# Kernel optimization log

Hardware: AMD Instinct MI355X
Metric: run time of the kernel (lower is better)

Reference implementation:

```python
import jax, jax.numpy as jnp
import numpy as np

NHEAD = 8
DILATED = 1


def setup_inputs() -> dict:
    key = jax.random.key(0)
    ks = jax.random.split(key, 5)
    bs, c, h, w, k = 2, 256, 128, 128, 8
    L = (h // 2) * (w // 2)
    return {
        "query": jax.random.normal(ks[0], (bs, c, h, w), jnp.float32),
        "key": jax.random.normal(ks[1], (bs, c, h, w), jnp.float32),
        "value": jax.random.normal(ks[2], (bs, c, h, w), jnp.float32),
        "topk_pos": jax.random.randint(ks[3], (bs, L, k, 2), 0, h // 2, dtype=jnp.int32).astype(jnp.int64),
        "rel_pos": jax.random.normal(ks[4], (bs, NHEAD, h, w, 4 * k), jnp.float32),
    }


def reference(query, key, value, topk_pos, rel_pos):
    bs, c, h0, w0 = query.shape
    h1, w1 = key.shape[2], key.shape[3]
    nh = NHEAD
    d = c // nh
    L = (h0 // 2) * (w0 // 2)
    k = topk_pos.shape[2]
    k4 = 4 * k

    # key/value: [b,c,h,w] -> [b, h1*w1, nh, d]
    kf = key.reshape(bs, c, h1 * w1).transpose(0, 2, 1).reshape(bs, h1 * w1, nh, d)
    vf = value.reshape(bs, c, h1 * w1).transpose(0, 2, 1).reshape(bs, h1 * w1, nh, d)

    # query grouped into 2x2 blocks: [b, L, 4, nh, d]
    q = query.reshape(bs, nh, d, h0 // 2, 2, w0 // 2, 2)
    q = q.transpose(0, 3, 5, 4, 6, 1, 2).reshape(bs, L, 4, nh, d)

    # build gather indices into flattened key grid (offsets by dilation)
    tp = topk_pos * 2                               # [b, L, k, 2]
    row, col = tp[..., 0], tp[..., 1]
    offs = [(0, 0), (0, DILATED), (DILATED, 0), (DILATED, DILATED)]
    idx = jnp.stack([(row + x) * w1 + (col + y) for x, y in offs], axis=3)  # [b,L,k,4]
    idx = jnp.clip(idx, 0, h1 * w1 - 1).reshape(bs, L, k4)

    def gather(tbl):  # tbl: [b, h1*w1, nh, d] -> [b, L, k4, nh, d]
        return jax.vmap(lambda t, i: t[i])(tbl, idx.reshape(bs, L * k4)).reshape(bs, L, k4, nh, d)

    kg = gather(kf)
    vg = gather(vf)

    scale = 1.0 / np.sqrt(d).astype(np.float32)
    qk = jnp.einsum('blthd,blmhd->bltmh', q, kg) * scale  # [b,L,4,k4,nh]

    rp = rel_pos.reshape(bs, nh, h0 // 2, 2, w0 // 2, 2, k4)
    rp = rp.transpose(0, 2, 4, 3, 5, 6, 1).reshape(bs, L, 4, k4, nh)
    qk = qk + rp

    A = jax.nn.softmax(qk, axis=-2)  # softmax over the k*4 candidate axis
    msg = jnp.einsum('bltmh,blmhd->blthd', A, vg)  # [b,L,4,nh,d]

    # un-group 2x2 blocks back to full resolution: [b, h0*w0, c]
    msg = msg.reshape(bs, h0 // 2, w0 // 2, 2, 2, nh, d)
    msg = msg.transpose(0, 1, 3, 2, 4, 5, 6).reshape(bs, h0 * w0, c)

    up_idx = jnp.broadcast_to(idx[:, :, None, :], (bs, L, 4, k4))
    up_idx = up_idx.reshape(bs, h0 // 2, w0 // 2, 2, 2, k4)
    up_idx = up_idx.transpose(0, 1, 3, 2, 4, 5).reshape(bs, h0 * w0, k4)
    return msg, up_idx
```

## Files before the change

kernel.cpp:

```cpp
#include <hip/hip_runtime.h>
#include <math.h>

constexpr int NH = 8;
constexpr int D = 32;
constexpr int C = 256;
constexpr int H0 = 128;
constexpr int W0 = 128;
constexpr int PIX = H0 * W0;
constexpr int LBLK = 4096;
constexpr int K4 = 32;
constexpr int KST = 258;

__global__ __launch_bounds__(256) void transpose_qkv_kernel(
    const float* __restrict__ q, const float* __restrict__ k,
    const float* __restrict__ v, float* __restrict__ ws)
{
  __shared__ float tile[64][65];
  const int arr = blockIdx.z >> 1;
  const int b = blockIdx.z & 1;
  const float* src = (arr == 0 ? q : arr == 1 ? k : v) + (size_t)b * C * PIX;
  float* dst = ws + (size_t)arr * 2 * PIX * C + (size_t)b * PIX * C;

  const int p0 = blockIdx.x * 64;
  const int c0 = blockIdx.y * 64;
  const int tx = threadIdx.x & 63;
  const int ty = threadIdx.x >> 6;

#pragma unroll
  for (int r = 0; r < 16; ++r) {
    const int ch = ty + r * 4;
    tile[ch][tx] = src[(size_t)(c0 + ch) * PIX + p0 + tx];
  }
  __syncthreads();
#pragma unroll
  for (int r = 0; r < 16; ++r) {
    const int prow = ty + r * 4;
    dst[(size_t)(p0 + prow) * C + c0 + tx] = tile[tx][prow];
  }
}

__global__ __launch_bounds__(256) void cascade_attn_kernel(
    const float* __restrict__ qT,
    const float* __restrict__ kT,
    const float* __restrict__ vT,
    const int* __restrict__ topk,
    const float* __restrict__ relp,
    float* __restrict__ out_msg,
    float* __restrict__ out_idx)
{
  __shared__ float kv[K4 * KST];
  __shared__ float qs[4 * C];
  __shared__ float as_[NH * K4 * 4];

  const int tid = threadIdx.x;
  const int bid = blockIdx.x;
  const int b = bid >> 12;
  const int l = bid & (LBLK - 1);
  const int by = l >> 6, bx = l & 63;
  const int r0 = by * 2, c0 = bx * 2;

  const int* tp = topk + ((size_t)b * LBLK + l) * 16;

  {
    const int t = tid >> 6, ln = tid & 63;
    const int pix = r0 * W0 + c0 + (t >> 1) * W0 + (t & 1);
    float4 f = *(const float4*)&qT[((size_t)b * PIX + pix) * C + ln * 4];
    *(float4*)&qs[t * C + ln * 4] = f;
  }

  const int p = tid >> 3;
  const int ln8 = tid & 7;
  const int jj = p >> 2, o = p & 3;
  const int gpix = (tp[jj * 2] * 2 + (o >> 1)) * W0 + tp[jj * 2 + 1] * 2 + (o & 1);

  {
    const float* src = &kT[((size_t)b * PIX + gpix) * C + ln8 * 4];
#pragma unroll
    for (int i = 0; i < 8; ++i) {
      float4 f = *(const float4*)(src + i * 32);
      float* dst = &kv[p * KST + ln8 * 4 + i * 32];
      ((float2*)dst)[0] = make_float2(f.x, f.y);
      ((float2*)(dst + 2))[0] = make_float2(f.z, f.w);
    }
  }

  float4 vreg[8];
  {
    const float* src = &vT[((size_t)b * PIX + gpix) * C + ln8 * 4];
#pragma unroll
    for (int i = 0; i < 8; ++i) vreg[i] = *(const float4*)(src + i * 32);
  }

  if (tid < 128) {
    const int m = tid & 31, t = tid >> 5;
    const int j2 = m >> 2, o2 = m & 3;
    const int pix = (tp[j2 * 2] * 2 + (o2 >> 1)) * W0 + tp[j2 * 2 + 1] * 2 + (o2 & 1);
    const int prow = r0 + (t >> 1), pcol = c0 + (t & 1);
    out_idx[((size_t)b * PIX + prow * W0 + pcol) * K4 + m] = (float)pix;
  }
  __syncthreads();

  const int h = tid >> 5;
  const int m = tid & 31;

  float a0 = 0.f, a1 = 0.f, a2 = 0.f, a3 = 0.f;
#pragma unroll
  for (int dq = 0; dq < 8; ++dq) {
    const int off = h * D + dq * 4;
    float4 q0 = *(const float4*)&qs[0 * C + off];
    float4 q1 = *(const float4*)&qs[1 * C + off];
    float4 q2 = *(const float4*)&qs[2 * C + off];
    float4 q3 = *(const float4*)&qs[3 * C + off];
    float2 ka = *(const float2*)&kv[m * KST + off];
    float2 kc = *(const float2*)&kv[m * KST + off + 2];
    a0 += q0.x * ka.x + q0.y * ka.y + q0.z * kc.x + q0.w * kc.y;
    a1 += q1.x * ka.x + q1.y * ka.y + q1.z * kc.x + q1.w * kc.y;
    a2 += q2.x * ka.x + q2.y * ka.y + q2.z * kc.x + q2.w * kc.y;
    a3 += q3.x * ka.x + q3.y * ka.y + q3.z * kc.x + q3.w * kc.y;
  }

  const float scale = 0.17677669529663687f;
  const size_t rb = ((((size_t)b * NH + h) * H0 + r0) * W0 + c0) * K4 + m;
  float sv[4];
  sv[0] = a0 * scale + relp[rb];
  sv[1] = a1 * scale + relp[rb + K4];
  sv[2] = a2 * scale + relp[rb + (size_t)W0 * K4];
  sv[3] = a3 * scale + relp[rb + (size_t)W0 * K4 + K4];

  float pr4[4];
#pragma unroll
  for (int t = 0; t < 4; ++t) {
    float x = sv[t];
    float mx = x;
#pragma unroll
    for (int off = 16; off > 0; off >>= 1) mx = fmaxf(mx, __shfl_xor(mx, off));
    float pbit = __expf(x - mx);
    float sm = pbit;
#pragma unroll
    for (int off = 16; off > 0; off >>= 1) sm += __shfl_xor(sm, off);
    pr4[t] = pbit / sm;
  }
  *(float4*)&as_[tid * 4] = make_float4(pr4[0], pr4[1], pr4[2], pr4[3]);
  __syncthreads();

#pragma unroll
  for (int i = 0; i < 8; ++i) {
    float* dst = &kv[p * KST + ln8 * 4 + i * 32];
    ((float2*)dst)[0] = make_float2(vreg[i].x, vreg[i].y);
    ((float2*)(dst + 2))[0] = make_float2(vreg[i].z, vreg[i].w);
  }
  __syncthreads();

  float o0 = 0.f, o1 = 0.f, o2 = 0.f, o3 = 0.f;
#pragma unroll
  for (int mm = 0; mm < 32; ++mm) {
    float4 a4 = *(const float4*)&as_[(h * K4 + mm) * 4];
    float vv = kv[mm * KST + h * D + m];
    o0 += a4.x * vv;
    o1 += a4.y * vv;
    o2 += a4.z * vv;
    o3 += a4.w * vv;
  }
  const size_t ob = ((size_t)b * PIX + (size_t)r0 * W0 + c0) * C + h * D + m;
  out_msg[ob] = o0;
  out_msg[ob + C] = o1;
  out_msg[ob + (size_t)W0 * C] = o2;
  out_msg[ob + (size_t)W0 * C + C] = o3;
}

__global__ __launch_bounds__(256) void cascade_attn_fallback(
    const float* __restrict__ query, const float* __restrict__ key,
    const float* __restrict__ value, const int* __restrict__ topk,
    const float* __restrict__ relp, float* __restrict__ out_msg,
    float* __restrict__ out_idx)
{
  __shared__ float kv[K4 * KST];
  __shared__ float qs[4 * C];
  __shared__ float as_[NH * K4 * 4];

  const int tid = threadIdx.x;
  const int bid = blockIdx.x;
  const int b = bid >> 12;
  const int l = bid & (LBLK - 1);
  const int by = l >> 6, bx = l & 63;
  const int r0 = by * 2, c0 = bx * 2;

  const size_t plane = (size_t)PIX;
  const float* qb = query + (size_t)b * C * plane;
  const float* kb = key + (size_t)b * C * plane;
  const float* vb = value + (size_t)b * C * plane;
  const int* tp = topk + ((size_t)b * LBLK + l) * 16;

  {
    const float* qp = qb + (size_t)tid * plane + r0 * W0 + c0;
    float2 a = *(const float2*)qp;
    float2 bb = *(const float2*)(qp + W0);
    qs[0 * C + tid] = a.x; qs[1 * C + tid] = a.y;
    qs[2 * C + tid] = bb.x; qs[3 * C + tid] = bb.y;
  }
#pragma unroll
  for (int it = 0; it < 16; ++it) {
    const int jj = it >> 1, x = it & 1;
    const int pr = tp[jj * 2] * 2 + x;
    const int pc = tp[jj * 2 + 1] * 2;
    float2 f = *(const float2*)(kb + (size_t)tid * plane + pr * W0 + pc);
    const int m0 = jj * 4 + x * 2;
    kv[m0 * KST + tid] = f.x;
    kv[(m0 + 1) * KST + tid] = f.y;
  }
  if (tid < 128) {
    const int m = tid & 31, t = tid >> 5;
    const int jj = m >> 2, o = m & 3;
    const int pix = (tp[jj * 2] * 2 + (o >> 1)) * W0 + tp[jj * 2 + 1] * 2 + (o & 1);
    const int prow = r0 + (t >> 1), pcol = c0 + (t & 1);
    out_idx[((size_t)b * plane + prow * W0 + pcol) * K4 + m] = (float)pix;
  }
  __syncthreads();

  const int h = tid >> 5;
  const int m = tid & 31;
  float a0 = 0.f, a1 = 0.f, a2 = 0.f, a3 = 0.f;
#pragma unroll
  for (int dq = 0; dq < 8; ++dq) {
    const int off = h * D + dq * 4;
    float4 q0 = *(const float4*)&qs[0 * C + off];
    float4 q1 = *(const float4*)&qs[1 * C + off];
    float4 q2 = *(const float4*)&qs[2 * C + off];
    float4 q3 = *(const float4*)&qs[3 * C + off];
    float2 ka = *(const float2*)&kv[m * KST + off];
    float2 kc = *(const float2*)&kv[m * KST + off + 2];
    a0 += q0.x * ka.x + q0.y * ka.y + q0.z * kc.x + q0.w * kc.y;
    a1 += q1.x * ka.x + q1.y * ka.y + q1.z * kc.x + q1.w * kc.y;
    a2 += q2.x * ka.x + q2.y * ka.y + q2.z * kc.x + q2.w * kc.y;
    a3 += q3.x * ka.x + q3.y * ka.y + q3.z * kc.x + q3.w * kc.y;
  }
  const float scale = 0.17677669529663687f;
  const size_t rb = ((((size_t)b * NH + h) * H0 + r0) * W0 + c0) * K4 + m;
  float sv[4];
  sv[0] = a0 * scale + relp[rb];
  sv[1] = a1 * scale + relp[rb + K4];
  sv[2] = a2 * scale + relp[rb + (size_t)W0 * K4];
  sv[3] = a3 * scale + relp[rb + (size_t)W0 * K4 + K4];
  float pr4[4];
#pragma unroll
  for (int t = 0; t < 4; ++t) {
    float x = sv[t];
    float mx = x;
#pragma unroll
    for (int off = 16; off > 0; off >>= 1) mx = fmaxf(mx, __shfl_xor(mx, off));
    float pbit = __expf(x - mx);
    float sm = pbit;
#pragma unroll
    for (int off = 16; off > 0; off >>= 1) sm += __shfl_xor(sm, off);
    pr4[t] = pbit / sm;
  }
  *(float4*)&as_[tid * 4] = make_float4(pr4[0], pr4[1], pr4[2], pr4[3]);
  __syncthreads();
#pragma unroll
  for (int it = 0; it < 16; ++it) {
    const int jj = it >> 1, x = it & 1;
    const int pr = tp[jj * 2] * 2 + x;
    const int pc = tp[jj * 2 + 1] * 2;
    float2 f = *(const float2*)(vb + (size_t)tid * plane + pr * W0 + pc);
    const int m0 = jj * 4 + x * 2;
    kv[m0 * KST + tid] = f.x;
    kv[(m0 + 1) * KST + tid] = f.y;
  }
  __syncthreads();
  float o0 = 0.f, o1 = 0.f, o2 = 0.f, o3 = 0.f;
#pragma unroll
  for (int mm = 0; mm < 32; ++mm) {
    float4 a4 = *(const float4*)&as_[(h * K4 + mm) * 4];
    float vv = kv[mm * KST + h * D + m];
    o0 += a4.x * vv; o1 += a4.y * vv; o2 += a4.z * vv; o3 += a4.w * vv;
  }
  const size_t ob = ((size_t)b * plane + (size_t)r0 * W0 + c0) * C + h * D + m;
  out_msg[ob] = o0;
  out_msg[ob + C] = o1;
  out_msg[ob + (size_t)W0 * C] = o2;
  out_msg[ob + (size_t)W0 * C + C] = o3;
}

extern "C" void kernel_launch(void* const* d_in, const int* in_sizes, int n_in,
                              void* d_out, int out_size, void* d_ws, size_t ws_size,
                              hipStream_t stream) {
  const float* q = (const float*)d_in[0];
  const float* k = (const float*)d_in[1];
  const float* v = (const float*)d_in[2];
  const int* tp = (const int*)d_in[3];
  const float* rp = (const float*)d_in[4];

  float* out_msg = (float*)d_out;
  float* out_idx = out_msg + (size_t)2 * PIX * C;

  const size_t needed = (size_t)3 * 2 * PIX * C * sizeof(float);
  if (ws_size >= needed) {
    float* ws = (float*)d_ws;
    float* qT = ws;
    float* kT = ws + (size_t)2 * PIX * C;
    float* vT = ws + (size_t)4 * PIX * C;
    dim3 tg(PIX / 64, C / 64, 6);
    hipLaunchKernelGGL(transpose_qkv_kernel, tg, dim3(256), 0, stream, q, k, v, ws);
    hipLaunchKernelGGL(cascade_attn_kernel, dim3(2 * LBLK), dim3(256), 0, stream,
                       qT, kT, vT, tp, rp, out_msg, out_idx);
  } else {
    hipLaunchKernelGGL(cascade_attn_fallback, dim3(2 * LBLK), dim3(256), 0, stream,
                       q, k, v, tp, rp, out_msg, out_idx);
  }
}
```

Baseline: 247.7 us.

## Vectorize transpose with float4, prefetch rel_pos early, reuse query smem for probs

The transpose kernel now moves data with float4 global loads and stores and scatters them into a padded shared tile, cutting the number of memory instructions. In the attention kernel the rel_pos loads are issued before the first barrier so their latency overlaps the K/V gathers. The softmax probabilities now overwrite the query shared buffer instead of using a separate array, which lowers shared memory per block and may raise occupancy. The transpose scatter writes into shared memory may incur bank conflicts, and the strided scalar reads of the tile are assembled into float4 stores.

```diff
diff --git a/kernel.cpp b/kernel.cpp
--- a/kernel.cpp
+++ b/kernel.cpp
@@ -15,7 +15,7 @@
     const float* __restrict__ q, const float* __restrict__ k,
     const float* __restrict__ v, float* __restrict__ ws)
 {
-  __shared__ float tile[64][65];
+  __shared__ float tile[64 * 65];
   const int arr = blockIdx.z >> 1;
   const int b = blockIdx.z & 1;
   const float* src = (arr == 0 ? q : arr == 1 ? k : v) + (size_t)b * C * PIX;
@@ -23,19 +23,27 @@
 
   const int p0 = blockIdx.x * 64;
   const int c0 = blockIdx.y * 64;
-  const int tx = threadIdx.x & 63;
-  const int ty = threadIdx.x >> 6;
-
-#pragma unroll
-  for (int r = 0; r < 16; ++r) {
-    const int ch = ty + r * 4;
-    tile[ch][tx] = src[(size_t)(c0 + ch) * PIX + p0 + tx];
-  }
-  __syncthreads();
-#pragma unroll
-  for (int r = 0; r < 16; ++r) {
-    const int prow = ty + r * 4;
-    dst[(size_t)(p0 + prow) * C + c0 + tx] = tile[tx][prow];
+  const int t15 = threadIdx.x & 15;
+  const int thi = threadIdx.x >> 4;
+
+#pragma unroll
+  for (int r = 0; r < 4; ++r) {
+    const int ch = thi + r * 16;
+    const int p4 = t15 * 4;
+    float4 f = *(const float4*)&src[(size_t)(c0 + ch) * PIX + p0 + p4];
+    tile[(p4 + 0) * 65 + ch] = f.x;
+    tile[(p4 + 1) * 65 + ch] = f.y;
+    tile[(p4 + 2) * 65 + ch] = f.z;
+    tile[(p4 + 3) * 65 + ch] = f.w;
+  }
+  __syncthreads();
+#pragma unroll
+  for (int r = 0; r < 4; ++r) {
+    const int p = thi + r * 16;
+    const int c4 = t15 * 4;
+    const float* tr = &tile[p * 65 + c4];
+    float4 g = make_float4(tr[0], tr[1], tr[2], tr[3]);
+    *(float4*)&dst[(size_t)(p0 + p) * C + c0 + c4] = g;
   }
 }
 
@@ -49,8 +57,7 @@
     float* __restrict__ out_idx)
 {
   __shared__ float kv[K4 * KST];
-  __shared__ float qs[4 * C];
-  __shared__ float as_[NH * K4 * 4];
+  __shared__ float qa[4 * C];
 
   const int tid = threadIdx.x;
   const int bid = blockIdx.x;
@@ -61,11 +68,14 @@
 
   const int* tp = topk + ((size_t)b * LBLK + l) * 16;
 
+  const int h = tid >> 5;
+  const int m = tid & 31;
+
   {
     const int t = tid >> 6, ln = tid & 63;
     const int pix = r0 * W0 + c0 + (t >> 1) * W0 + (t & 1);
     float4 f = *(const float4*)&qT[((size_t)b * PIX + pix) * C + ln * 4];
-    *(float4*)&qs[t * C + ln * 4] = f;
+    *(float4*)&qa[t * C + ln * 4] = f;
   }
 
   const int p = tid >> 3;
@@ -91,26 +101,29 @@
     for (int i = 0; i < 8; ++i) vreg[i] = *(const float4*)(src + i * 32);
   }
 
+  const size_t rb = ((((size_t)b * NH + h) * H0 + r0) * W0 + c0) * K4 + m;
+  float rl0 = relp[rb];
+  float rl1 = relp[rb + K4];
+  float rl2 = relp[rb + (size_t)W0 * K4];
+  float rl3 = relp[rb + (size_t)W0 * K4 + K4];
+
   if (tid < 128) {
-    const int m = tid & 31, t = tid >> 5;
-    const int j2 = m >> 2, o2 = m & 3;
+    const int mm = tid & 31, t = tid >> 5;
+    const int j2 = mm >> 2, o2 = mm & 3;
     const int pix = (tp[j2 * 2] * 2 + (o2 >> 1)) * W0 + tp[j2 * 2 + 1] * 2 + (o2 & 1);
     const int prow = r0 + (t >> 1), pcol = c0 + (t & 1);
-    out_idx[((size_t)b * PIX + prow * W0 + pcol) * K4 + m] = (float)pix;
-  }
-  __syncthreads();
-
-  const int h = tid >> 5;
-  const int m = tid & 31;
+    out_idx[((size_t)b * PIX + prow * W0 + pcol) * K4 + mm] = (float)pix;
+  }
+  __syncthreads();
 
   float a0 = 0.f, a1 = 0.f, a2 = 0.f, a3 = 0.f;
 #pragma unroll
   for (int dq = 0; dq < 8; ++dq) {
     const int off = h * D + dq * 4;
-    float4 q0 = *(const float4*)&qs[0 * C + off];
-    float4 q1 = *(const float4*)&qs[1 * C + off];
-    float4 q2 = *(const float4*)&qs[2 * C + off];
-    float4 q3 = *(const float4*)&qs[3 * C + off];
+    float4 q0 = *(const float4*)&qa[0 * C + off];
+    float4 q1 = *(const float4*)&qa[1 * C + off];
+    float4 q2 = *(const float4*)&qa[2 * C + off];
+    float4 q3 = *(const float4*)&qa[3 * C + off];
     float2 ka = *(const float2*)&kv[m * KST + off];
     float2 kc = *(const float2*)&kv[m * KST + off + 2];
     a0 += q0.x * ka.x + q0.y * ka.y + q0.z * kc.x + q0.w * kc.y;
@@ -120,12 +133,11 @@
   }
 
   const float scale = 0.17677669529663687f;
-  const size_t rb = ((((size_t)b * NH + h) * H0 + r0) * W0 + c0) * K4 + m;
   float sv[4];
-  sv[0] = a0 * scale + relp[rb];
-  sv[1] = a1 * scale + relp[rb + K4];
-  sv[2] = a2 * scale + relp[rb + (size_t)W0 * K4];
-  sv[3] = a3 * scale + relp[rb + (size_t)W0 * K4 + K4];
+  sv[0] = a0 * scale + rl0;
+  sv[1] = a1 * scale + rl1;
+  sv[2] = a2 * scale + rl2;
+  sv[3] = a3 * scale + rl3;
 
   float pr4[4];
 #pragma unroll
@@ -140,9 +152,9 @@
     for (int off = 16; off > 0; off >>= 1) sm += __shfl_xor(sm, off);
     pr4[t] = pbit / sm;
   }
-  *(float4*)&as_[tid * 4] = make_float4(pr4[0], pr4[1], pr4[2], pr4[3]);
-  __syncthreads();
-
+  __syncthreads();
+
+  *(float4*)&qa[tid * 4] = make_float4(pr4[0], pr4[1], pr4[2], pr4[3]);
 #pragma unroll
   for (int i = 0; i < 8; ++i) {
     float* dst = &kv[p * KST + ln8 * 4 + i * 32];
@@ -154,7 +166,7 @@
   float o0 = 0.f, o1 = 0.f, o2 = 0.f, o3 = 0.f;
 #pragma unroll
   for (int mm = 0; mm < 32; ++mm) {
-    float4 a4 = *(const float4*)&as_[(h * K4 + mm) * 4];
+    float4 a4 = *(const float4*)&qa[(h * K4 + mm) * 4];
     float vv = kv[mm * KST + h * D + m];
     o0 += a4.x * vv;
     o1 += a4.y * vv;
```

After: 240.9 us. 2.7% less time.
